# Optimization experiments

Measured on AMD Instinct MI355X. Metric: run time of the kernel, lower is better.

## Reference

```python
import jax, jax.numpy as jnp
import numpy as np

B, N, E, IN_DIM, OUT_DIM = 8, 4500, 72000, 128, 128
EPS = 1e-5  # torch LayerNorm default


def setup_inputs() -> dict:
    key = jax.random.key(0)
    k0, k1, k2 = jax.random.split(key, 3)
    node_features = jax.random.normal(k0, (B, N, IN_DIM), dtype=jnp.float32)
    edge_index = jax.random.randint(k1, (B, 2, E), 0, N, dtype=jnp.int64)
    node_mask = jnp.ones((B, N), dtype=jnp.float32)
    edge_mask = jnp.ones((B, E), dtype=jnp.float32)
    W = (jax.random.normal(k2, (OUT_DIM, IN_DIM), dtype=jnp.float32)
         / np.float32(np.sqrt(IN_DIM)))
    b = jnp.zeros((OUT_DIM,), dtype=jnp.float32)
    gamma = jnp.ones((OUT_DIM,), dtype=jnp.float32)
    beta = jnp.zeros((OUT_DIM,), dtype=jnp.float32)
    return {"node_features": node_features, "edge_index": edge_index,
            "node_mask": node_mask, "edge_mask": edge_mask,
            "W": W, "b": b, "gamma": gamma, "beta": beta}


def reference(node_features, edge_index, node_mask, edge_mask, W, b, gamma, beta):
    Bsz, Nn, _ = node_features.shape
    # linear transform: h = x W^T + b  -> [B, N, out_dim]
    h = jnp.einsum('bni,oi->bno', node_features, W) + b
    D = h.shape[-1]
    total = Bsz * Nn

    # With all nodes valid, the sparse index of node (b, n) is b*Nn + n.
    offsets = (jnp.arange(Bsz, dtype=edge_index.dtype) * Nn)[:, None]  # [B,1]
    src = (edge_index[:, 0, :] + offsets).reshape(-1)  # [B*E]
    tgt = (edge_index[:, 1, :] + offsets).reshape(-1)  # [B*E]
    ew = edge_mask.reshape(-1)                          # [B*E] edge validity

    flat_h = h.reshape(total, D)

    # in-degree (valid edges only) + self-loop, D^{-1/2} normalization
    deg = jax.ops.segment_sum(ew, tgt, num_segments=total) + 1.0
    dinv = deg ** -0.5

    coef = dinv[src] * dinv[tgt] * ew                   # [B*E]
    msg = flat_h[src] * coef[:, None]                   # gather + weight
    agg = jax.ops.segment_sum(msg, tgt, num_segments=total)
    agg = agg + flat_h * dinv[:, None]                  # self contribution

    h = h + agg.reshape(Bsz, Nn, D)                     # residual

    # dropout is identity at inference; LayerNorm then ReLU then mask
    mu = jnp.mean(h, axis=-1, keepdims=True)
    var = jnp.mean((h - mu) ** 2, axis=-1, keepdims=True)
    h = (h - mu) / jnp.sqrt(var + EPS) * gamma + beta
    h = jax.nn.relu(h) * node_mask[..., None]
    return h
```

## Files before the change

kernel.cpp:

```cpp
#include <hip/hip_runtime.h>
#include <math.h>

typedef unsigned short ushort_t;
typedef unsigned int uint_t;
typedef __attribute__((ext_vector_type(8))) short bf16x8;
typedef __attribute__((ext_vector_type(16))) float f32x16;

constexpr int Bc   = 8;
constexpr int Nn   = 4500;
constexpr int Ec   = 72000;
constexpr int D    = 128;
constexpr int T    = Bc * Nn;
constexpr int TE   = Bc * Ec;
constexpr float EPS = 1e-5f;

constexpr int PAD = 32;
constexpr int RST = 64;

constexpr int NB_W    = 64;
constexpr int NB_Z    = (T * PAD / 4) / 256;
constexpr int NB_X    = (T * D / 4) / 256;
constexpr int NB_PREP = NB_W + NB_Z + NB_X;

constexpr int NB_ECH  = (Ec + 255) / 256;
constexpr int NB_EDGE = 8 * NB_ECH;

constexpr size_t WS_CNTP  = 0;
constexpr size_t WS_EDATA = 4608000;
constexpr size_t WS_DINV  = 13824000;
constexpr size_t WS_XHI   = 13968000;
constexpr size_t WS_XLO   = 23184000;
constexpr size_t WS_WHI   = 32400000;
constexpr size_t WS_WLO   = 32432768;
constexpr size_t WS_H     = 32465536;

__device__ __forceinline__ ushort_t f32_to_bf16_rne(float f) {
  uint_t u = __float_as_uint(f);
  uint_t r = (u + 0x7fffu + ((u >> 16) & 1u)) >> 16;
  return (ushort_t)r;
}
__device__ __forceinline__ float bf16_to_f32(ushort_t h) {
  return __uint_as_float(((uint_t)h) << 16);
}

__global__ __launch_bounds__(256) void prep_kernel(
    const float* __restrict__ W, ushort_t* __restrict__ Whi,
    ushort_t* __restrict__ Wlo, int4* __restrict__ cntp4,
    const float* __restrict__ x, ushort_t* __restrict__ xhi,
    ushort_t* __restrict__ xlo) {
  const int bid = blockIdx.x;
  if (bid < NB_W) {
    int i = bid * 256 + threadIdx.x;
    float w = W[i];
    ushort_t hi = f32_to_bf16_rne(w);
    Whi[i] = hi;
    Wlo[i] = f32_to_bf16_rne(w - bf16_to_f32(hi));
  } else if (bid < NB_W + NB_Z) {
    int i = (bid - NB_W) * 256 + threadIdx.x;
    cntp4[i] = make_int4(0, 0, 0, 0);
  } else {
    int i = (bid - NB_W - NB_Z) * 256 + threadIdx.x;
    float4 v = ((const float4*)x)[i];
    ushort4 hi, lo;
    hi.x = f32_to_bf16_rne(v.x); lo.x = f32_to_bf16_rne(v.x - bf16_to_f32(hi.x));
    hi.y = f32_to_bf16_rne(v.y); lo.y = f32_to_bf16_rne(v.y - bf16_to_f32(hi.y));
    hi.z = f32_to_bf16_rne(v.z); lo.z = f32_to_bf16_rne(v.z - bf16_to_f32(hi.z));
    hi.w = f32_to_bf16_rne(v.w); lo.w = f32_to_bf16_rne(v.w - bf16_to_f32(hi.w));
    ((ushort4*)xhi)[i] = hi;
    ((ushort4*)xlo)[i] = lo;
  }
}

__global__ __launch_bounds__(256) void edge_kernel(
    const int* __restrict__ ei, const float* __restrict__ em,
    int* __restrict__ cntp, uint_t* __restrict__ edata) {
  const int b  = blockIdx.x & 7;
  const int el = (blockIdx.x >> 3) * 256 + threadIdx.x;
  if (el >= Ec) return;
  const int* eb = ei + b * 2 * Ec;
  int t0 = eb[Ec + el];
  if ((unsigned)t0 >= (unsigned)Nn) return;
  int tg = t0 + b * Nn;
  int rk = atomicAdd(&cntp[(size_t)tg * PAD], 1);
  if (rk >= RST) return;
  int s0 = eb[el];
  float ew = em[b * Ec + el];
  uint_t sl = (uint_t)s0;
  if ((unsigned)s0 >= (unsigned)Nn) { sl = 0; ew = 0.f; }
  uint_t pk = ((uint_t)f32_to_bf16_rne(ew) << 16) | sl;
  edata[(size_t)tg * RST + rk] = pk;
}

__global__ __launch_bounds__(256) void dinv_kernel(
    const uint_t* __restrict__ edata, const int* __restrict__ cntp,
    float* __restrict__ dinv) {
  int i = blockIdx.x * 256 + threadIdx.x;
  if (i >= T) return;
  int cnt = cntp[(size_t)i * PAD];
  cnt = (cnt > RST) ? RST : cnt;
  const uint_t* row = edata + (size_t)i * RST;
  float s = 0.f;
  for (int j = 0; j < cnt; ++j) s += bf16_to_f32((ushort_t)(row[j] >> 16));
  dinv[i] = 1.0f / sqrtf(s + 1.0f);
}

__global__ __launch_bounds__(256) void gemm_kernel(
    const ushort_t* __restrict__ xhi, const ushort_t* __restrict__ xlo,
    const ushort_t* __restrict__ Whi, const ushort_t* __restrict__ Wlo,
    const float* __restrict__ bias, float* __restrict__ h) {
  const int wid  = threadIdx.x >> 6;
  const int lane = threadIdx.x & 63;
  const int m0 = blockIdx.x * 32;
  const int r  = lane & 31;
  const int kh = lane >> 5;

  const size_t arow = (size_t)(m0 + r) * D + kh * 8;

  f32x16 acc;
#pragma unroll
  for (int j = 0; j < 16; ++j) acc[j] = 0.f;

#pragma unroll
  for (int ks = 0; ks < 8; ++ks) {
    bf16x8 ahi = *(const bf16x8*)(xhi + arow + ks * 16);
    bf16x8 alo = *(const bf16x8*)(xlo + arow + ks * 16);
    const size_t boff = (size_t)(wid * 32 + r) * D + ks * 16 + kh * 8;
    bf16x8 bhi = *(const bf16x8*)(Whi + boff);
    bf16x8 blo = *(const bf16x8*)(Wlo + boff);
    acc = __builtin_amdgcn_mfma_f32_32x32x16_bf16(ahi, bhi, acc, 0, 0, 0);
    acc = __builtin_amdgcn_mfma_f32_32x32x16_bf16(ahi, blo, acc, 0, 0, 0);
    acc = __builtin_amdgcn_mfma_f32_32x32x16_bf16(alo, bhi, acc, 0, 0, 0);
  }

  const int col = wid * 32 + r;
  const float bv = bias[col];
#pragma unroll
  for (int j = 0; j < 16; ++j) {
    const int mrow = m0 + (j & 3) + 8 * (j >> 2) + 4 * kh;
    h[(size_t)mrow * D + col] = acc[j] + bv;
  }
}

__global__ __launch_bounds__(256) void gather_ln_kernel(
    const float* __restrict__ h, const int* __restrict__ cntp,
    const uint_t* __restrict__ edata, const float* __restrict__ dinv,
    const float* __restrict__ gamma, const float* __restrict__ beta,
    const float* __restrict__ mask, float* __restrict__ out) {
  const int bid  = blockIdx.x;
  const int b    = bid & 7;
  const int wid  = threadIdx.x >> 6;
  const int node = b * Nn + (bid >> 3) * 4 + wid;
  const int bOff = b * Nn;
  const int lane = threadIdx.x & 63;
  const int f4   = lane & 31;
  const int half = lane >> 5;

  const float4* h4 = (const float4*)h;
  int cnt = cntp[(size_t)node * PAD];
  cnt = (cnt > RST) ? RST : cnt;
  const uint_t* row = edata + (size_t)node * RST;

  float4 hv = h4[(size_t)node * 32 + f4];

  float4 accE = make_float4(0.f, 0.f, 0.f, 0.f);
  int i = half;
  for (; i + 6 < cnt; i += 8) {
    uint_t p0 = row[i];
    uint_t p1 = row[i + 2];
    uint_t p2 = row[i + 4];
    uint_t p3 = row[i + 6];
    int sg0 = bOff + (p0 & 0xFFFFu);
    int sg1 = bOff + (p1 & 0xFFFFu);
    int sg2 = bOff + (p2 & 0xFFFFu);
    int sg3 = bOff + (p3 & 0xFFFFu);
    float c0 = dinv[sg0] * bf16_to_f32((ushort_t)(p0 >> 16));
    float c1 = dinv[sg1] * bf16_to_f32((ushort_t)(p1 >> 16));
    float c2 = dinv[sg2] * bf16_to_f32((ushort_t)(p2 >> 16));
    float c3 = dinv[sg3] * bf16_to_f32((ushort_t)(p3 >> 16));
    float4 v0 = h4[(size_t)sg0 * 32 + f4];
    float4 v1 = h4[(size_t)sg1 * 32 + f4];
    float4 v2 = h4[(size_t)sg2 * 32 + f4];
    float4 v3 = h4[(size_t)sg3 * 32 + f4];
    accE.x += v0.x * c0 + v1.x * c1 + v2.x * c2 + v3.x * c3;
    accE.y += v0.y * c0 + v1.y * c1 + v2.y * c2 + v3.y * c3;
    accE.z += v0.z * c0 + v1.z * c1 + v2.z * c2 + v3.z * c3;
    accE.w += v0.w * c0 + v1.w * c1 + v2.w * c2 + v3.w * c3;
  }
  for (; i < cnt; i += 2) {
    uint_t p0 = row[i];
    int sg0 = bOff + (p0 & 0xFFFFu);
    float c0 = dinv[sg0] * bf16_to_f32((ushort_t)(p0 >> 16));
    float4 v0 = h4[(size_t)sg0 * 32 + f4];
    accE.x += v0.x * c0;
    accE.y += v0.y * c0;
    accE.z += v0.z * c0;
    accE.w += v0.w * c0;
  }

  accE.x += __shfl_xor(accE.x, 32);
  accE.y += __shfl_xor(accE.y, 32);
  accE.z += __shfl_xor(accE.z, 32);
  accE.w += __shfl_xor(accE.w, 32);

  const float dt = dinv[node];
  float4 acc;
  acc.x = hv.x * (1.f + dt) + dt * accE.x;
  acc.y = hv.y * (1.f + dt) + dt * accE.y;
  acc.z = hv.z * (1.f + dt) + dt * accE.z;
  acc.w = hv.w * (1.f + dt) + dt * accE.w;

  float su = acc.x + acc.y + acc.z + acc.w;
  float ss = acc.x * acc.x + acc.y * acc.y + acc.z * acc.z + acc.w * acc.w;
#pragma unroll
  for (int o = 16; o > 0; o >>= 1) {
    su += __shfl_xor(su, o);
    ss += __shfl_xor(ss, o);
  }
  float mu  = su * (1.0f / 128.0f);
  float var = ss * (1.0f / 128.0f) - mu * mu;
  float rs  = 1.0f / sqrtf(var + EPS);
  float m   = mask[node];

  float4 g  = ((const float4*)gamma)[f4];
  float4 bb = ((const float4*)beta)[f4];
  float4 rv;
  rv.x = fmaxf((acc.x - mu) * rs * g.x + bb.x, 0.f) * m;
  rv.y = fmaxf((acc.y - mu) * rs * g.y + bb.y, 0.f) * m;
  rv.z = fmaxf((acc.z - mu) * rs * g.z + bb.z, 0.f) * m;
  rv.w = fmaxf((acc.w - mu) * rs * g.w + bb.w, 0.f) * m;
  if (half == 0) ((float4*)out)[(size_t)node * 32 + f4] = rv;
}

extern "C" void kernel_launch(void* const* d_in, const int* in_sizes, int n_in,
                              void* d_out, int out_size, void* d_ws, size_t ws_size,
                              hipStream_t stream) {
  const float* x     = (const float*)d_in[0];
  const int*   ei    = (const int*)d_in[1];
  const float* nmask = (const float*)d_in[2];
  const float* emask = (const float*)d_in[3];
  const float* W     = (const float*)d_in[4];
  const float* bias  = (const float*)d_in[5];
  const float* gamma = (const float*)d_in[6];
  const float* beta  = (const float*)d_in[7];
  float* out = (float*)d_out;

  char*     ws    = (char*)d_ws;
  int*      cntp  = (int*)     (ws + WS_CNTP);
  uint_t*   edata = (uint_t*)  (ws + WS_EDATA);
  float*    dinv  = (float*)   (ws + WS_DINV);
  ushort_t* xhi   = (ushort_t*)(ws + WS_XHI);
  ushort_t* xlo   = (ushort_t*)(ws + WS_XLO);
  ushort_t* Whi   = (ushort_t*)(ws + WS_WHI);
  ushort_t* Wlo   = (ushort_t*)(ws + WS_WLO);
  float*    h     = (float*)   (ws + WS_H);

  prep_kernel<<<NB_PREP, 256, 0, stream>>>(W, Whi, Wlo, (int4*)cntp, x, xhi, xlo);
  edge_kernel<<<NB_EDGE, 256, 0, stream>>>(ei, emask, cntp, edata);
  dinv_kernel<<<(T + 255) / 256, 256, 0, stream>>>(edata, cntp, dinv);
  gemm_kernel<<<T / 32, 256, 0, stream>>>(xhi, xlo, Whi, Wlo, bias, h);
  gather_ln_kernel<<<T / 4, 256, 0, stream>>>(h, cntp, edata, dinv,
                                              gamma, beta, nmask, out);
}
```

Measured before the change: 90.93 us.

## Fuse x bf16 hi/lo split into GEMM and give each wave two column tiles

Drops the separate pass in the prep kernel that split x into bf16 hi/lo halves in workspace. The GEMM now loads fp32 x directly and converts it in registers. Each wave now computes two 32-column output tiles, so every converted A fragment feeds six MFMAs instead of three. This removes a write and re-read of about 18 MB of intermediate data, but x rows are now loaded twice (once per column half), and the wave holds two accumulators, which raises register pressure.

Result: faster. 87.53 us (-3.7%).

```diff
diff --git a/kernel.cpp b/kernel.cpp
--- a/kernel.cpp
+++ b/kernel.cpp
@@ -19,20 +19,19 @@
 
 constexpr int NB_W    = 64;
 constexpr int NB_Z    = (T * PAD / 4) / 256;
-constexpr int NB_X    = (T * D / 4) / 256;
-constexpr int NB_PREP = NB_W + NB_Z + NB_X;
+constexpr int NB_PREP = NB_W + NB_Z;
 
 constexpr int NB_ECH  = (Ec + 255) / 256;
 constexpr int NB_EDGE = 8 * NB_ECH;
+
+constexpr int NB_GEMM = ((T / 32) * 2 + 3) / 4;
 
 constexpr size_t WS_CNTP  = 0;
 constexpr size_t WS_EDATA = 4608000;
 constexpr size_t WS_DINV  = 13824000;
-constexpr size_t WS_XHI   = 13968000;
-constexpr size_t WS_XLO   = 23184000;
-constexpr size_t WS_WHI   = 32400000;
-constexpr size_t WS_WLO   = 32432768;
-constexpr size_t WS_H     = 32465536;
+constexpr size_t WS_WHI   = 13968000;
+constexpr size_t WS_WLO   = 14000768;
+constexpr size_t WS_H     = 14033536;
 
 __device__ __forceinline__ ushort_t f32_to_bf16_rne(float f) {
   uint_t u = __float_as_uint(f);
@@ -45,9 +44,7 @@
 
 __global__ __launch_bounds__(256) void prep_kernel(
     const float* __restrict__ W, ushort_t* __restrict__ Whi,
-    ushort_t* __restrict__ Wlo, int4* __restrict__ cntp4,
-    const float* __restrict__ x, ushort_t* __restrict__ xhi,
-    ushort_t* __restrict__ xlo) {
+    ushort_t* __restrict__ Wlo, int4* __restrict__ cntp4) {
   const int bid = blockIdx.x;
   if (bid < NB_W) {
     int i = bid * 256 + threadIdx.x;
@@ -55,19 +52,9 @@
     ushort_t hi = f32_to_bf16_rne(w);
     Whi[i] = hi;
     Wlo[i] = f32_to_bf16_rne(w - bf16_to_f32(hi));
-  } else if (bid < NB_W + NB_Z) {
+  } else {
     int i = (bid - NB_W) * 256 + threadIdx.x;
     cntp4[i] = make_int4(0, 0, 0, 0);
-  } else {
-    int i = (bid - NB_W - NB_Z) * 256 + threadIdx.x;
-    float4 v = ((const float4*)x)[i];
-    ushort4 hi, lo;
-    hi.x = f32_to_bf16_rne(v.x); lo.x = f32_to_bf16_rne(v.x - bf16_to_f32(hi.x));
-    hi.y = f32_to_bf16_rne(v.y); lo.y = f32_to_bf16_rne(v.y - bf16_to_f32(hi.y));
-    hi.z = f32_to_bf16_rne(v.z); lo.z = f32_to_bf16_rne(v.z - bf16_to_f32(hi.z));
-    hi.w = f32_to_bf16_rne(v.w); lo.w = f32_to_bf16_rne(v.w - bf16_to_f32(hi.w));
-    ((ushort4*)xhi)[i] = hi;
-    ((ushort4*)xlo)[i] = lo;
   }
 }
 
@@ -105,39 +92,58 @@
 }
 
 __global__ __launch_bounds__(256) void gemm_kernel(
-    const ushort_t* __restrict__ xhi, const ushort_t* __restrict__ xlo,
-    const ushort_t* __restrict__ Whi, const ushort_t* __restrict__ Wlo,
-    const float* __restrict__ bias, float* __restrict__ h) {
-  const int wid  = threadIdx.x >> 6;
+    const float* __restrict__ x, const ushort_t* __restrict__ Whi,
+    const ushort_t* __restrict__ Wlo, const float* __restrict__ bias,
+    float* __restrict__ h) {
+  const int g = blockIdx.x * 4 + (threadIdx.x >> 6);
+  if (g >= (T / 32) * 2) return;
   const int lane = threadIdx.x & 63;
-  const int m0 = blockIdx.x * 32;
+  const int mt = g >> 1;
+  const int nh = g & 1;
+  const int m0 = mt * 32;
   const int r  = lane & 31;
   const int kh = lane >> 5;
 
-  const size_t arow = (size_t)(m0 + r) * D + kh * 8;
-
-  f32x16 acc;
-#pragma unroll
-  for (int j = 0; j < 16; ++j) acc[j] = 0.f;
+  const float* xrow = x + (size_t)(m0 + r) * D + kh * 8;
+
+  f32x16 acc[2];
+#pragma unroll
+  for (int n = 0; n < 2; ++n)
+#pragma unroll
+    for (int j = 0; j < 16; ++j) acc[n][j] = 0.f;
 
 #pragma unroll
   for (int ks = 0; ks < 8; ++ks) {
-    bf16x8 ahi = *(const bf16x8*)(xhi + arow + ks * 16);
-    bf16x8 alo = *(const bf16x8*)(xlo + arow + ks * 16);
-    const size_t boff = (size_t)(wid * 32 + r) * D + ks * 16 + kh * 8;
-    bf16x8 bhi = *(const bf16x8*)(Whi + boff);
-    bf16x8 blo = *(const bf16x8*)(Wlo + boff);
-    acc = __builtin_amdgcn_mfma_f32_32x32x16_bf16(ahi, bhi, acc, 0, 0, 0);
-    acc = __builtin_amdgcn_mfma_f32_32x32x16_bf16(ahi, blo, acc, 0, 0, 0);
-    acc = __builtin_amdgcn_mfma_f32_32x32x16_bf16(alo, bhi, acc, 0, 0, 0);
-  }
-
-  const int col = wid * 32 + r;
-  const float bv = bias[col];
-#pragma unroll
-  for (int j = 0; j < 16; ++j) {
-    const int mrow = m0 + (j & 3) + 8 * (j >> 2) + 4 * kh;
-    h[(size_t)mrow * D + col] = acc[j] + bv;
+    const float4 p0 = ((const float4*)(xrow + ks * 16))[0];
+    const float4 p1 = ((const float4*)(xrow + ks * 16))[1];
+    const float xa[8] = {p0.x, p0.y, p0.z, p0.w, p1.x, p1.y, p1.z, p1.w};
+    bf16x8 ahi, alo;
+#pragma unroll
+    for (int j = 0; j < 8; ++j) {
+      ushort_t hb = f32_to_bf16_rne(xa[j]);
+      ahi[j] = (short)hb;
+      alo[j] = (short)f32_to_bf16_rne(xa[j] - bf16_to_f32(hb));
+    }
+#pragma unroll
+    for (int n = 0; n < 2; ++n) {
+      const size_t boff = (size_t)((nh * 2 + n) * 32 + r) * D + ks * 16 + kh * 8;
+      bf16x8 bhi = *(const bf16x8*)(Whi + boff);
+      bf16x8 blo = *(const bf16x8*)(Wlo + boff);
+      acc[n] = __builtin_amdgcn_mfma_f32_32x32x16_bf16(ahi, bhi, acc[n], 0, 0, 0);
+      acc[n] = __builtin_amdgcn_mfma_f32_32x32x16_bf16(ahi, blo, acc[n], 0, 0, 0);
+      acc[n] = __builtin_amdgcn_mfma_f32_32x32x16_bf16(alo, bhi, acc[n], 0, 0, 0);
+    }
+  }
+
+#pragma unroll
+  for (int n = 0; n < 2; ++n) {
+    const int col = (nh * 2 + n) * 32 + r;
+    const float bv = bias[col];
+#pragma unroll
+    for (int j = 0; j < 16; ++j) {
+      const int mrow = m0 + (j & 3) + 8 * (j >> 2) + 4 * kh;
+      h[(size_t)mrow * D + col] = acc[n][j] + bv;
+    }
   }
 }
 
@@ -248,16 +254,14 @@
   int*      cntp  = (int*)     (ws + WS_CNTP);
   uint_t*   edata = (uint_t*)  (ws + WS_EDATA);
   float*    dinv  = (float*)   (ws + WS_DINV);
-  ushort_t* xhi   = (ushort_t*)(ws + WS_XHI);
-  ushort_t* xlo   = (ushort_t*)(ws + WS_XLO);
   ushort_t* Whi   = (ushort_t*)(ws + WS_WHI);
   ushort_t* Wlo   = (ushort_t*)(ws + WS_WLO);
   float*    h     = (float*)   (ws + WS_H);
 
-  prep_kernel<<<NB_PREP, 256, 0, stream>>>(W, Whi, Wlo, (int4*)cntp, x, xhi, xlo);
+  prep_kernel<<<NB_PREP, 256, 0, stream>>>(W, Whi, Wlo, (int4*)cntp);
   edge_kernel<<<NB_EDGE, 256, 0, stream>>>(ei, emask, cntp, edata);
   dinv_kernel<<<(T + 255) / 256, 256, 0, stream>>>(edata, cntp, dinv);
-  gemm_kernel<<<T / 32, 256, 0, stream>>>(xhi, xlo, Whi, Wlo, bias, h);
+  gemm_kernel<<<NB_GEMM, 256, 0, stream>>>(x, Whi, Wlo, bias, h);
   gather_ln_kernel<<<T / 4, 256, 0, stream>>>(h, cntp, edata, dinv,
                                               gamma, beta, nmask, out);
 }
```
